# Kernel optimization log

Measured on AMD Instinct MI355X. Metric: run time of the kernel, lower is better.

Reference implementation:

```python
import jax, jax.numpy as jnp
import numpy as np

B, L, D = 4, 2048, 1024
H, DK, DV = 4, 256, 256
CHUNK = 32
MIN_FLOOR, MAX_FLOOR = 0.01, 0.1
EPS = 1e-5


def _l2norm(x):
    return x * jax.lax.rsqrt(jnp.sum(x * x, -1, keepdims=True) + 1e-6)


def _causal_dwconv(x, w):
    # x: [b, L, C], w: [C, k] -> depthwise causal 1d conv
    b, l, c = x.shape
    k = w.shape[-1]
    xt = jnp.transpose(x, (0, 2, 1))
    y = jax.lax.conv_general_dilated(xt, w[:, None, :], (1,), [(k - 1, 0)],
                                     dimension_numbers=('NCH', 'OIH', 'NCH'),
                                     feature_group_count=c)
    return jnp.transpose(y, (0, 2, 1))


def _delta_rule_chunkwise(q, k, v, beta, chunk=CHUNK):
    # q,k: [b,h,L,dk]; v: [b,h,L,dv]; beta: [b,h,L]; L % chunk == 0
    b, h, l, dk = q.shape
    dv = v.shape[-1]
    q = _l2norm(q)
    k = _l2norm(k)
    v = v * beta[..., None]
    kb = k * beta[..., None]
    n = l // chunk
    resh = lambda t: t.reshape(b, h, n, chunk, t.shape[-1])
    q, k, v, kb = resh(q), resh(k), resh(v), resh(kb)
    tri = jnp.triu(jnp.ones((chunk, chunk), bool))        # incl diag
    strict = jnp.triu(jnp.ones((chunk, chunk), bool), 1)  # excl diag
    att = jnp.where(tri, 0.0, -(kb @ jnp.swapaxes(k, -1, -2)))
    # UT transform: forward substitution building (I - lower)^{-1}
    for i in range(1, chunk):
        upd = jnp.einsum('bhnj,bhnjk->bhnk', att[..., i, :], att)
        att = att.at[..., i, :i].add(upd[..., :i])
    att = att + jnp.eye(chunk, dtype=att.dtype)
    u = att @ v
    w = att @ kb

    def step(S, xs):
        q_i, k_i, u_i, w_i = xs  # [b,h,chunk,d]
        local = jnp.where(strict, 0.0, q_i @ jnp.swapaxes(k_i, -1, -2))
        u_adj = u_i - w_i @ S
        o_i = q_i @ S + local @ u_adj
        return S + jnp.swapaxes(k_i, -1, -2) @ u_adj, o_i

    xs = tuple(jnp.moveaxis(t, 2, 0) for t in (q, k, u, w))
    S0 = jnp.zeros((b, h, dk, dv), q.dtype)
    S, o = jax.lax.scan(step, S0, xs)
    return jnp.moveaxis(o, 0, 2).reshape(b, h, l, dv), S


def _rmsnorm(x, w):
    return x * jax.lax.rsqrt(jnp.mean(x * x, -1, keepdims=True) + EPS) * w


def setup_inputs():
    key = jax.random.key(0)
    ks = jax.random.split(key, 16)
    s = 0.02
    return {
        'hidden_states': jax.random.normal(ks[0], (B, L, D), jnp.float32),
        'W_q': jax.random.normal(ks[1], (D, H * DK), jnp.float32) * s,
        'W_k': jax.random.normal(ks[2], (D, H * DK), jnp.float32) * s,
        'W_v': jax.random.normal(ks[3], (D, H * DV), jnp.float32) * s,
        'W_b': jax.random.normal(ks[4], (D, H), jnp.float32) * s,
        'conv_w_q': jax.random.normal(ks[5], (H * DK, 4), jnp.float32) * 0.3,
        'conv_w_k': jax.random.normal(ks[6], (H * DK, 4), jnp.float32) * 0.3,
        'conv_w_v': jax.random.normal(ks[7], (H * DV, 4), jnp.float32) * 0.3,
        'fir_short_w': jax.random.normal(ks[8], (H, DV, 3), jnp.float32) * 0.1,
        'fir_long_w': jax.random.normal(ks[9], (H, DV, 31), jnp.float32) * 0.1,
        'W_fuse1': jax.random.normal(ks[10], (D + 3 * H * DV, 2 * D), jnp.float32) * s,
        'b_fuse1': jnp.zeros((2 * D,), jnp.float32),
        'W_fuse2': jax.random.normal(ks[11], (2 * D, H * 4), jnp.float32) * s,
        'b_fuse2': jnp.zeros((H * 4,), jnp.float32).at[3::4].set(4.0),
        'others_log_tau': jnp.zeros((H,), jnp.float32),
        'norm_w': jnp.ones((DV,), jnp.float32),
        'W_o': jax.random.normal(ks[12], (H * DV, D), jnp.float32) * s,
    }


def reference(hidden_states, W_q, W_k, W_v, W_b, conv_w_q, conv_w_k, conv_w_v,
              fir_short_w, fir_long_w, W_fuse1, b_fuse1, W_fuse2, b_fuse2,
              others_log_tau, norm_w, W_o):
    b, l, d = hidden_states.shape
    # projections + mandatory short conv (silu activation)
    q = jax.nn.silu(_causal_dwconv(hidden_states @ W_q, conv_w_q))
    k = jax.nn.silu(_causal_dwconv(hidden_states @ W_k, conv_w_k))
    v = jax.nn.silu(_causal_dwconv(hidden_states @ W_v, conv_w_v))
    q = q.reshape(b, l, H, DK)
    k = k.reshape(b, l, H, DK)
    v = v.reshape(b, l, H, DV)
    beta = jax.nn.sigmoid(hidden_states @ W_b)  # [b,l,H]
    delta_out, _ = _delta_rule_chunkwise(
        jnp.transpose(q, (0, 2, 1, 3)), jnp.transpose(k, (0, 2, 1, 3)),
        jnp.transpose(v, (0, 2, 1, 3)), jnp.transpose(beta, (0, 2, 1)))
    delta_out = jnp.transpose(delta_out, (0, 2, 1, 3))  # [b,l,H,DV]
    # depthwise FIR paths on v
    vc = v.reshape(b, l, H * DV)
    fir_s = _causal_dwconv(vc, fir_short_w.reshape(H * DV, -1)).reshape(b, l, H, DV)
    fir_l = _causal_dwconv(vc, fir_long_w.reshape(H * DV, -1)).reshape(b, l, H, DV)
    # fusion gate MLP
    gate_in = jnp.concatenate([hidden_states, fir_s.reshape(b, l, -1),
                               fir_l.reshape(b, l, -1), delta_out.reshape(b, l, -1)], -1)
    hid = jax.nn.gelu(gate_in @ W_fuse1 + b_fuse1, approximate=False)
    logits = (hid @ W_fuse2 + b_fuse2).reshape(b, l, H, 4)
    p_raw = jax.nn.sigmoid(logits[..., 3])
    # token-adaptive context floor
    floor = MIN_FLOOR + (MAX_FLOOR - MIN_FLOOR) * (1.0 - p_raw)
    p_val = (1.0 - floor) * p_raw
    tau = jnp.exp(others_log_tau)  # per-head temperature
    others = jax.nn.softmax(logits[..., :3] / tau[None, None, :, None], -1)
    p_ctx = (1.0 - p_val)[..., None] * others
    o = (p_ctx[..., 0:1] * fir_s + p_ctx[..., 1:2] * fir_l +
         p_ctx[..., 2:3] * delta_out + p_val[..., None] * v)
    o = _rmsnorm(o, norm_w)
    return o.reshape(b, l, H * DV) @ W_o
```

## Files before the change

kernel.cpp:

```cpp
#include <hip/hip_runtime.h>
#include <hip/hip_bf16.h>

#define B_ 4
#define L_ 2048
#define D_ 1024
#define H_ 4
#define DK_ 256
#define DV_ 256
#define NCH 64
#define NTOK 8192

typedef __attribute__((ext_vector_type(8))) short bf16x8;
typedef __attribute__((ext_vector_type(4))) float f32x4;
typedef unsigned int u32;

__device__ __forceinline__ float bu2f(unsigned short u) {
    union { unsigned int i; float f; } x; x.i = ((unsigned int)u) << 16; return x.f;
}
__device__ __forceinline__ unsigned short f2bu(float f) {
    union { __hip_bfloat16 h; unsigned short u; } x; x.h = __float2bfloat16(f); return x.u;
}
#define MFMA16(a, b, c) __builtin_amdgcn_mfma_f32_16x16x32_bf16(a, b, c, 0, 0, 0)

__device__ __forceinline__ void gload16(const void* g, void* l) {
    __builtin_amdgcn_global_load_lds(
        (const __attribute__((address_space(1))) u32*)g,
        (__attribute__((address_space(3))) u32*)l, 16, 0, 0);
}

__global__ __launch_bounds__(256) void k_transpose(const float* __restrict__ in,
                                                   unsigned short* __restrict__ out,
                                                   int K, int N) {
    __shared__ float tile[32][33];
    int k0 = blockIdx.y * 32, n0 = blockIdx.x * 32;
    int tx = threadIdx.x & 31, ty = threadIdx.x >> 5;
#pragma unroll
    for (int r = 0; r < 4; ++r)
        tile[ty + 8 * r][tx] = in[(long)(k0 + ty + 8 * r) * N + n0 + tx];
    __syncthreads();
#pragma unroll
    for (int r = 0; r < 4; ++r)
        out[(long)(n0 + ty + 8 * r) * K + k0 + tx] = f2bu(tile[tx][ty + 8 * r]);
}

__global__ __launch_bounds__(256) void k_padT2(const float* __restrict__ W,
                                               unsigned short* __restrict__ out) {
    long idx = (long)blockIdx.x * 256 + threadIdx.x;
    int n = (int)(idx >> 11), k = (int)(idx & 2047);
    out[idx] = (n < 16) ? f2bu(W[k * 16 + n]) : (unsigned short)0;
}

__global__ __launch_bounds__(256) void k_cvt_hs(const float4* __restrict__ hs4,
                                                unsigned short* __restrict__ gate_in) {
    int idx = blockIdx.x * 256 + threadIdx.x;
    float4 v = hs4[idx];
    int row = idx >> 8;
    int c4 = (idx & 255) * 4;
    ushort4 o;
    o.x = f2bu(v.x); o.y = f2bu(v.y); o.z = f2bu(v.z); o.w = f2bu(v.w);
    *reinterpret_cast<ushort4*>(&gate_in[(long)row * 4096 + c4]) = o;
}

__global__ __launch_bounds__(64) void k_beta(const float* __restrict__ hs,
                                             const float* __restrict__ W_b,
                                             float* __restrict__ beta) {
    int tok = blockIdx.x;
    int lane = threadIdx.x;
    const float* hrow = hs + (long)tok * D_;
    float acc0 = 0, acc1 = 0, acc2 = 0, acc3 = 0;
    for (int c = lane; c < D_; c += 64) {
        float x = hrow[c];
        float4 wb = reinterpret_cast<const float4*>(W_b)[c];
        acc0 += x * wb.x; acc1 += x * wb.y; acc2 += x * wb.z; acc3 += x * wb.w;
    }
#pragma unroll
    for (int off = 32; off; off >>= 1) {
        acc0 += __shfl_down(acc0, off);
        acc1 += __shfl_down(acc1, off);
        acc2 += __shfl_down(acc2, off);
        acc3 += __shfl_down(acc3, off);
    }
    if (lane == 0) {
        int b = tok >> 11, l = tok & 2047;
        beta[((long)(b * H_ + 0)) * L_ + l] = 1.f / (1.f + expf(-acc0));
        beta[((long)(b * H_ + 1)) * L_ + l] = 1.f / (1.f + expf(-acc1));
        beta[((long)(b * H_ + 2)) * L_ + l] = 1.f / (1.f + expf(-acc2));
        beta[((long)(b * H_ + 3)) * L_ + l] = 1.f / (1.f + expf(-acc3));
    }
}

template <int EPI>
__global__ __launch_bounds__(256) void k_gemm(const unsigned short* __restrict__ A, int lda,
                                              const unsigned short* __restrict__ BT, int ldb,
                                              void* __restrict__ Cout, int ldc,
                                              const float* __restrict__ bias,
                                              int K, int gx) {
    __shared__ __align__(16) unsigned short As[128][64];
    __shared__ __align__(16) unsigned short Bs[128][64];
    const int tid = threadIdx.x;
    const int wave = tid >> 6, lane = tid & 63;
    const int wm = wave & 1, wn = wave >> 1;
    const int lr = lane & 15, lg = lane >> 4;
    const int nwg = gridDim.x;
    const int cpx = nwg >> 3;
    const int orig = blockIdx.x;
    const int wg = (orig & 7) * cpx + (orig >> 3);
    const int m0 = (wg / gx) * 128, n0 = (wg % gx) * 128;
    const int srow = wave * 32 + (lane >> 3);
    const int scol = (lane & 7) * 8;
    const unsigned short* Ap = &A[(long)(m0 + srow) * lda + scol];
    const unsigned short* Bp = &BT[(long)(n0 + srow) * ldb + scol];
    unsigned short* AsB = &As[wave * 32][0];
    unsigned short* BsB = &Bs[wave * 32][0];
    f32x4 acc[4][4] = {};
    for (int k0 = 0; k0 < K; k0 += 64) {
#pragma unroll
        for (int g = 0; g < 4; ++g) {
            gload16(Ap + (long)g * 8 * lda + k0, AsB + g * 8 * 64);
            gload16(Bp + (long)g * 8 * ldb + k0, BsB + g * 8 * 64);
        }
        __syncthreads();
#pragma unroll
        for (int ks = 0; ks < 2; ++ks) {
            bf16x8 af[4], bfr[4];
#pragma unroll
            for (int mt = 0; mt < 4; ++mt)
                af[mt] = *reinterpret_cast<const bf16x8*>(&As[wm * 64 + mt * 16 + lr][ks * 32 + lg * 8]);
#pragma unroll
            for (int nt = 0; nt < 4; ++nt)
                bfr[nt] = *reinterpret_cast<const bf16x8*>(&Bs[wn * 64 + nt * 16 + lr][ks * 32 + lg * 8]);
#pragma unroll
            for (int mt = 0; mt < 4; ++mt)
#pragma unroll
                for (int nt = 0; nt < 4; ++nt)
                    acc[mt][nt] = MFMA16(af[mt], bfr[nt], acc[mt][nt]);
        }
        __syncthreads();
    }
#pragma unroll
    for (int mt = 0; mt < 4; ++mt)
#pragma unroll
        for (int nt = 0; nt < 4; ++nt)
#pragma unroll
            for (int r = 0; r < 4; ++r) {
                int row = m0 + wm * 64 + mt * 16 + lg * 4 + r;
                int col = n0 + wn * 64 + nt * 16 + lr;
                float v = acc[mt][nt][r];
                if (EPI == 2) {
                    v += bias[col];
                    v = 0.5f * v * (1.f + erff(v * 0.70710678118f));
                }
                if (EPI == 0)
                    reinterpret_cast<float*>(Cout)[(long)row * ldc + col] = v;
                else
                    reinterpret_cast<unsigned short*>(Cout)[(long)row * ldc + col] = f2bu(v);
            }
}

__global__ __launch_bounds__(256) void k_conv_silu(const unsigned short* __restrict__ QKVp,
                                                   const float* __restrict__ cwq,
                                                   const float* __restrict__ cwk,
                                                   const float* __restrict__ cwv,
                                                   unsigned short* __restrict__ qn,
                                                   unsigned short* __restrict__ kn,
                                                   unsigned short* __restrict__ v_blc) {
    int tok = blockIdx.x;
    int b = tok >> 11, l = tok & 2047;
    int t = threadIdx.x;
    float y[12];
#pragma unroll
    for (int j = 0; j < 12; ++j) {
        int c = t + 256 * j;
        const float* cw = (j < 4) ? &cwq[c * 4] : (j < 8) ? &cwk[(c - 1024) * 4] : &cwv[(c - 2048) * 4];
        float s = 0.f;
#pragma unroll
        for (int jj = 0; jj < 4; ++jj) {
            int tl = l - 3 + jj;
            if (tl >= 0) s += bu2f(QKVp[((long)(b * L_ + tl)) * 3072 + c]) * cw[jj];
        }
        y[j] = s / (1.f + expf(-s));
    }
    float sq[8];
#pragma unroll
    for (int j = 0; j < 8; ++j) sq[j] = y[j] * y[j];
    int wave = t >> 6, lane = t & 63;
#pragma unroll
    for (int off = 32; off; off >>= 1)
#pragma unroll
        for (int j = 0; j < 8; ++j) sq[j] += __shfl_down(sq[j], off);
    __shared__ float red[4][8];
    if (lane == 0)
#pragma unroll
        for (int j = 0; j < 8; ++j) red[wave][j] = sq[j];
    __syncthreads();
    float tot[8];
#pragma unroll
    for (int j = 0; j < 8; ++j) tot[j] = red[0][j] + red[1][j] + red[2][j] + red[3][j];
#pragma unroll
    for (int h = 0; h < 4; ++h) {
        float sc = rsqrtf(tot[h] + 1e-6f);
        qn[((long)(b * H_ + h) * L_ + l) * 256 + t] = f2bu(y[h] * sc);
    }
#pragma unroll
    for (int h = 0; h < 4; ++h) {
        float sc = rsqrtf(tot[4 + h] + 1e-6f);
        kn[((long)(b * H_ + h) * L_ + l) * 256 + t] = f2bu(y[4 + h] * sc);
    }
#pragma unroll
    for (int h = 0; h < 4; ++h)
        v_blc[(long)tok * 1024 + h * 256 + t] = f2bu(y[8 + h]);
}

__global__ __launch_bounds__(256) void k_delta_chunk(const unsigned short* __restrict__ qn,
                                                     const unsigned short* __restrict__ kn,
                                                     const unsigned short* __restrict__ v_blc,
                                                     const float* __restrict__ beta,
                                                     unsigned short* __restrict__ u_buf,
                                                     unsigned short* __restrict__ w_buf,
                                                     unsigned short* __restrict__ local_buf,
                                                     unsigned short* __restrict__ kT_buf) {
    int bid = blockIdx.x;
    int n = bid & 63, bh = bid >> 6;
    int b = bh >> 2, h = bh & 3;
    int t0 = n * 32;
    __shared__ __align__(16) unsigned short k_s[32][264];
    __shared__ __align__(16) unsigned short vbT[256][40];
    __shared__ __align__(16) unsigned short kbT[256][40];
    __shared__ __align__(16) float att[32][33];
    __shared__ __align__(16) unsigned short att_b[32][40];
    __shared__ float bet[32];
    int tid = threadIdx.x, wave = tid >> 6, lane = tid & 63;
    int lr = lane & 15, lg = lane >> 4;

    {
        int row = tid >> 3;
        int cc = (tid & 7) * 32;
        float brow = beta[(long)bh * L_ + t0 + row];
        if ((tid & 7) == 0) bet[row] = brow;
        const uint4* kp = reinterpret_cast<const uint4*>(&kn[((long)bh * L_ + t0 + row) * 256 + cc]);
        const uint4* vp = reinterpret_cast<const uint4*>(&v_blc[((long)(b * L_ + t0 + row)) * 1024 + h * 256 + cc]);
        unsigned short kv[32], vv[32];
#pragma unroll
        for (int g = 0; g < 4; ++g) {
            uint4 x = kp[g];
            *reinterpret_cast<uint4*>(&kv[g * 8]) = x;
            *reinterpret_cast<uint4*>(&k_s[row][cc + g * 8]) = x;
            *reinterpret_cast<uint4*>(&vv[g * 8]) = vp[g];
        }
#pragma unroll
        for (int e = 0; e < 32; ++e) {
            kbT[cc + e][row] = f2bu(bu2f(kv[e]) * brow);
            vbT[cc + e][row] = f2bu(bu2f(vv[e]) * brow);
        }
    }
    __syncthreads();

    {
        unsigned short tmp[32];
#pragma unroll
        for (int t = 0; t < 32; ++t) tmp[t] = k_s[t][tid];
#pragma unroll
        for (int g = 0; g < 4; ++g)
            *reinterpret_cast<uint4*>(&kT_buf[((long)bid * 256 + tid) * 32 + g * 8]) =
                *reinterpret_cast<uint4*>(&tmp[g * 8]);
    }

    {
        int i0 = (wave & 1) * 16, j0 = (wave >> 1) * 16;
        f32x4 G = {0, 0, 0, 0}, S2 = {0, 0, 0, 0};
#pragma unroll
        for (int kk = 0; kk < 8; ++kk) {
            bf16x8 bk = *reinterpret_cast<const bf16x8*>(&k_s[j0 + lr][kk * 32 + lg * 8]);
            bf16x8 ak = *reinterpret_cast<const bf16x8*>(&k_s[i0 + lr][kk * 32 + lg * 8]);
            bf16x8 aq = *reinterpret_cast<const bf16x8*>(&qn[((long)bh * L_ + t0 + i0 + lr) * 256 + kk * 32 + lg * 8]);
            G = MFMA16(ak, bk, G);
            S2 = MFMA16(aq, bk, S2);
        }
#pragma unroll
        for (int r = 0; r < 4; ++r) {
            int i = i0 + lg * 4 + r, j = j0 + lr;
            att[i][j] = (j < i) ? -bet[i] * G[r] : 0.f;
            local_buf[(long)bid * 1024 + i * 32 + j] = f2bu((j <= i) ? S2[r] : 0.f);
        }
    }
    __syncthreads();

    for (int i = 1; i < 32; ++i) {
        float upd = 0.f;
        if (tid < i) {
            for (int j = tid + 1; j < i; ++j) upd += att[i][j] * att[j][tid];
        }
        __syncthreads();
        if (tid < i) att[i][tid] += upd;
        __syncthreads();
    }
    for (int e = tid; e < 1024; e += 256) {
        int i = e >> 5, j = e & 31;
        att_b[i][j] = f2bu(att[i][j] + ((i == j) ? 1.f : 0.f));
    }
    __syncthreads();

    {
        int mt = wave & 1;
        bf16x8 afr = *reinterpret_cast<const bf16x8*>(&att_b[mt * 16 + lr][lg * 8]);
        f32x4 z = {0, 0, 0, 0};
#pragma unroll
        for (int ntt = 0; ntt < 8; ++ntt) {
            int n0c = (wave >> 1) * 128 + ntt * 16;
            bf16x8 bu = *reinterpret_cast<const bf16x8*>(&vbT[n0c + lr][lg * 8]);
            bf16x8 bw = *reinterpret_cast<const bf16x8*>(&kbT[n0c + lr][lg * 8]);
            f32x4 ut = MFMA16(afr, bu, z);
            f32x4 wt = MFMA16(afr, bw, z);
#pragma unroll
            for (int r = 0; r < 4; ++r) {
                int t = mt * 16 + lg * 4 + r, c = n0c + lr;
                u_buf[((long)bid * 32 + t) * 256 + c] = f2bu(ut[r]);
                w_buf[((long)bid * 32 + t) * 256 + c] = f2bu(wt[r]);
            }
        }
    }
}

__global__ __launch_bounds__(256) void k_scan(const unsigned short* __restrict__ qn,
                                              const unsigned short* __restrict__ u_buf,
                                              const unsigned short* __restrict__ w_buf,
                                              const unsigned short* __restrict__ local_buf,
                                              const unsigned short* __restrict__ kT_buf,
                                              unsigned short* __restrict__ gate_in) {
    int bid = blockIdx.x;
    int bh = bid & 15, dvb = bid >> 4;
    int b = bh >> 2, h = bh & 3;
    int dc0 = dvb * 16;
    __shared__ __align__(16) unsigned short Tb[16][264];
    __shared__ __align__(16) unsigned short uaT[16][40];
    const int tid = threadIdx.x, wave = tid >> 6, lane = tid & 63;
    const int lr = lane & 15, lg = lane >> 4;
    const int wi = wave & 1;
    const bool isW = wave < 2;
    const int c0w = wave * 64;
    f32x4 Tacc[4] = {};
    for (int e = tid; e < 16 * 264; e += 256) (&Tb[0][0])[e] = 0;
    const unsigned short* q_bh = qn + (long)bh * L_ * 256;
    const unsigned short* u_bh = u_buf + (long)bh * 64 * 8192;
    const unsigned short* w_bh = w_buf + (long)bh * 64 * 8192;
    const unsigned short* l_bh = local_buf + (long)bh * 64 * 1024;
    const unsigned short* kT_bh = kT_buf + (long)bh * 64 * 8192;
    const unsigned short* wq_base = (isW ? w_bh : q_bh) + (16 * wi + lr) * 256;
    const unsigned short* u_base = u_bh + (16 * wi + lg * 4) * 256 + dc0 + lr;
    const unsigned short* l_base = l_bh + (16 * wi + lr) * 32 + lg * 8;
    const unsigned short* kT_base = kT_bh + (c0w + lr) * 32 + lg * 8;
    bf16x8 wqA[8], kB[4], lA = {};
    float uv[4];
    auto prefetch = [&](int n) {
        long o8 = (long)n * 8192;
#pragma unroll
        for (int kk = 0; kk < 8; ++kk)
            wqA[kk] = *reinterpret_cast<const bf16x8*>(wq_base + o8 + kk * 32 + lg * 8);
#pragma unroll
        for (int cc = 0; cc < 4; ++cc)
            kB[cc] = *reinterpret_cast<const bf16x8*>(kT_base + o8 + cc * 512);
        if (isW) {
#pragma unroll
            for (int r = 0; r < 4; ++r) uv[r] = bu2f(u_base[o8 + r * 256]);
        } else {
            lA = *reinterpret_cast<const bf16x8*>(l_base + (long)n * 1024);
        }
    };
    prefetch(0);
    __syncthreads();
    for (int n = 0; n < 64; ++n) {
        f32x4 P0 = {0, 0, 0, 0}, P1 = {0, 0, 0, 0};
#pragma unroll
        for (int kk = 0; kk < 8; kk += 2) {
            bf16x8 t0 = *reinterpret_cast<const bf16x8*>(&Tb[lr][kk * 32 + lg * 8]);
            bf16x8 t1 = *reinterpret_cast<const bf16x8*>(&Tb[lr][(kk + 1) * 32 + lg * 8]);
            P0 = MFMA16(wqA[kk], t0, P0);
            P1 = MFMA16(wqA[kk + 1], t1, P1);
        }
        f32x4 P;
#pragma unroll
        for (int r = 0; r < 4; ++r) P[r] = P0[r] + P1[r];
        if (isW) {
#pragma unroll
            for (int r = 0; r < 4; ++r)
                uaT[lr][16 * wi + lg * 4 + r] = f2bu(uv[r] - P[r]);
        }
        bf16x8 kBc[4];
#pragma unroll
        for (int cc = 0; cc < 4; ++cc) kBc[cc] = kB[cc];
        bf16x8 lAc = lA;
        if (n + 1 < 64) prefetch(n + 1);
        __syncthreads();
        bf16x8 uaA = *reinterpret_cast<const bf16x8*>(&uaT[lr][lg * 8]);
        if (!isW) {
            f32x4 O = MFMA16(lAc, uaA, P);
#pragma unroll
            for (int r = 0; r < 4; ++r) {
                long row = (long)b * L_ + n * 32 + 16 * wi + lg * 4 + r;
                gate_in[row * 4096 + 3072 + h * 256 + dc0 + lr] = f2bu(O[r]);
            }
        }
#pragma unroll
        for (int cc = 0; cc < 4; ++cc)
            Tacc[cc] = MFMA16(uaA, kBc[cc], Tacc[cc]);
#pragma unroll
        for (int cc = 0; cc < 4; ++cc)
#pragma unroll
            for (int r = 0; r < 4; ++r)
                Tb[lg * 4 + r][c0w + cc * 16 + lr] = f2bu(Tacc[cc][r]);
        __syncthreads();
    }
}

__global__ __launch_bounds__(256) void k_fir(const unsigned short* __restrict__ v_blc,
                                             const float* __restrict__ ws3,
                                             const float* __restrict__ wl31,
                                             unsigned short* __restrict__ gate_in) {
    __shared__ unsigned short xs[94][256];
    int b = blockIdx.y, tt = blockIdx.x * 64, c0 = blockIdx.z * 256;
    int tid = threadIdx.x;
    for (int r = 0; r < 94; ++r) {
        int t = tt - 30 + r;
        xs[r][tid] = (t >= 0) ? v_blc[((long)(b * L_ + t)) * 1024 + c0 + tid] : (unsigned short)0;
    }
    int c = c0 + tid;
    float wl[31], ws[3];
#pragma unroll
    for (int j = 0; j < 31; ++j) wl[j] = wl31[(long)c * 31 + j];
#pragma unroll
    for (int j = 0; j < 3; ++j) ws[j] = ws3[(long)c * 3 + j];
    __syncthreads();
    for (int t = 0; t < 64; ++t) {
        float accl = 0.f, accs = 0.f;
#pragma unroll
        for (int j = 0; j < 31; ++j) accl += bu2f(xs[t + j][tid]) * wl[j];
#pragma unroll
        for (int j = 0; j < 3; ++j) accs += bu2f(xs[t + 28 + j][tid]) * ws[j];
        long row = (long)b * L_ + tt + t;
        gate_in[row * 4096 + 1024 + c] = f2bu(accs);
        gate_in[row * 4096 + 2048 + c] = f2bu(accl);
    }
}

__global__ __launch_bounds__(256) void k_gate(const float* __restrict__ logits_pre,
                                              const float* __restrict__ b_fuse2,
                                              const float* __restrict__ log_tau,
                                              const float* __restrict__ norm_w,
                                              const unsigned short* __restrict__ gate_in,
                                              const unsigned short* __restrict__ v_blc,
                                              unsigned short* __restrict__ o_norm) {
    int tok = blockIdx.x;
    int tid = threadIdx.x;
    __shared__ float lg_s[16];
    __shared__ float red[4][4];
    if (tid < 16) lg_s[tid] = logits_pre[(long)tok * 128 + tid] + b_fuse2[tid];
    __syncthreads();
    float o[4];
#pragma unroll
    for (int h = 0; h < 4; ++h) {
        float l0 = lg_s[h * 4 + 0], l1 = lg_s[h * 4 + 1], l2 = lg_s[h * 4 + 2], l3 = lg_s[h * 4 + 3];
        float praw = 1.f / (1.f + expf(-l3));
        float fl_ = 0.01f + 0.09f * (1.f - praw);
        float pval = (1.f - fl_) * praw;
        float itau = expf(-log_tau[h]);
        float a0 = l0 * itau, a1 = l1 * itau, a2 = l2 * itau;
        float m = fmaxf(a0, fmaxf(a1, a2));
        float e0 = expf(a0 - m), e1 = expf(a1 - m), e2 = expf(a2 - m);
        float inv = (1.f - pval) / (e0 + e1 + e2);
        long base = (long)tok * 4096;
        float fs = bu2f(gate_in[base + 1024 + h * 256 + tid]);
        float flv = bu2f(gate_in[base + 2048 + h * 256 + tid]);
        float dd = bu2f(gate_in[base + 3072 + h * 256 + tid]);
        float vv = bu2f(v_blc[(long)tok * 1024 + h * 256 + tid]);
        o[h] = e0 * inv * fs + e1 * inv * flv + e2 * inv * dd + pval * vv;
    }
    int wave = tid >> 6, lane = tid & 63;
    float s[4];
#pragma unroll
    for (int h = 0; h < 4; ++h) s[h] = o[h] * o[h];
#pragma unroll
    for (int off = 32; off; off >>= 1)
#pragma unroll
        for (int h = 0; h < 4; ++h) s[h] += __shfl_down(s[h], off);
    if (lane == 0)
#pragma unroll
        for (int h = 0; h < 4; ++h) red[wave][h] = s[h];
    __syncthreads();
#pragma unroll
    for (int h = 0; h < 4; ++h) {
        float tot = red[0][h] + red[1][h] + red[2][h] + red[3][h];
        float sc = rsqrtf(tot * (1.f / 256.f) + 1e-5f);
        o_norm[(long)tok * 1024 + h * 256 + tid] = f2bu(o[h] * sc * norm_w[tid]);
    }
}

extern "C" void kernel_launch(void* const* d_in, const int* in_sizes, int n_in,
                              void* d_out, int out_size, void* d_ws, size_t ws_size,
                              hipStream_t stream) {
    const float* hs = (const float*)d_in[0];
    const float* W_q = (const float*)d_in[1];
    const float* W_k = (const float*)d_in[2];
    const float* W_v = (const float*)d_in[3];
    const float* W_b = (const float*)d_in[4];
    const float* cwq = (const float*)d_in[5];
    const float* cwk = (const float*)d_in[6];
    const float* cwv = (const float*)d_in[7];
    const float* fir_s_w = (const float*)d_in[8];
    const float* fir_l_w = (const float*)d_in[9];
    const float* W_f1 = (const float*)d_in[10];
    const float* b_f1 = (const float*)d_in[11];
    const float* W_f2 = (const float*)d_in[12];
    const float* b_f2 = (const float*)d_in[13];
    const float* log_tau = (const float*)d_in[14];
    const float* norm_w = (const float*)d_in[15];
    const float* W_o = (const float*)d_in[16];

    char* ws = (char*)d_ws;
    size_t off = 0;
    auto alloc = [&](size_t bytes) { size_t o = off; off += (bytes + 255) & ~(size_t)255; return o; };
    unsigned short* gate_in = (unsigned short*)(ws + alloc((size_t)NTOK * 4096 * 2));
    unsigned short* QKVp    = (unsigned short*)(ws + alloc((size_t)NTOK * 3072 * 2));
    unsigned short* WqkvT   = (unsigned short*)(ws + alloc((size_t)3072 * 1024 * 2));
    unsigned short* Wf1T    = (unsigned short*)(ws + alloc((size_t)2048 * 4096 * 2));
    unsigned short* WoT     = (unsigned short*)(ws + alloc((size_t)1024 * 1024 * 2));
    unsigned short* Wf2Tp   = (unsigned short*)(ws + alloc((size_t)128 * 2048 * 2));
    float*          beta    = (float*)(ws + alloc((size_t)16 * 2048 * 4));
    unsigned short* qn      = (unsigned short*)(ws + alloc((size_t)16 * 2048 * 256 * 2));
    unsigned short* kn      = (unsigned short*)(ws + alloc((size_t)16 * 2048 * 256 * 2));
    unsigned short* v_blc   = (unsigned short*)(ws + alloc((size_t)NTOK * 1024 * 2));
    unsigned short* u_buf   = (unsigned short*)(ws + alloc((size_t)16 * 64 * 8192 * 2));
    unsigned short* w_buf   = (unsigned short*)(ws + alloc((size_t)16 * 64 * 8192 * 2));
    unsigned short* locb    = (unsigned short*)(ws + alloc((size_t)16 * 64 * 1024 * 2));
    unsigned short* kT_buf  = (unsigned short*)(ws + alloc((size_t)16 * 64 * 8192 * 2));
    float*          logits  = (float*)(ws + alloc((size_t)NTOK * 128 * 4));
    unsigned short* o_norm  = (unsigned short*)(ws + alloc((size_t)NTOK * 1024 * 2));
    unsigned short* hid     = QKVp;

    k_transpose<<<dim3(32, 32), 256, 0, stream>>>(W_q, WqkvT, 1024, 1024);
    k_transpose<<<dim3(32, 32), 256, 0, stream>>>(W_k, WqkvT + (size_t)1024 * 1024, 1024, 1024);
    k_transpose<<<dim3(32, 32), 256, 0, stream>>>(W_v, WqkvT + (size_t)2048 * 1024, 1024, 1024);
    k_transpose<<<dim3(64, 128), 256, 0, stream>>>(W_f1, Wf1T, 4096, 2048);
    k_transpose<<<dim3(32, 32), 256, 0, stream>>>(W_o, WoT, 1024, 1024);
    k_padT2<<<1024, 256, 0, stream>>>(W_f2, Wf2Tp);
    k_cvt_hs<<<8192, 256, 0, stream>>>((const float4*)hs, gate_in);
    k_beta<<<8192, 64, 0, stream>>>(hs, W_b, beta);
    k_gemm<1><<<24 * 64, 256, 0, stream>>>(gate_in, 4096, WqkvT, 1024, QKVp, 3072, nullptr,
                                           1024, 24);
    k_conv_silu<<<8192, 256, 0, stream>>>(QKVp, cwq, cwk, cwv, qn, kn, v_blc);
    k_delta_chunk<<<1024, 256, 0, stream>>>(qn, kn, v_blc, beta, u_buf, w_buf, locb, kT_buf);
    k_scan<<<256, 256, 0, stream>>>(qn, u_buf, w_buf, locb, kT_buf, gate_in);
    k_fir<<<dim3(32, 4, 4), 256, 0, stream>>>(v_blc, fir_s_w, fir_l_w, gate_in);
    k_gemm<2><<<16 * 64, 256, 0, stream>>>(gate_in, 4096, Wf1T, 4096, hid, 2048, b_f1,
                                           4096, 16);
    k_gemm<0><<<1 * 64, 256, 0, stream>>>(hid, 2048, Wf2Tp, 2048, logits, 128, nullptr,
                                          2048, 1);
    k_gate<<<8192, 256, 0, stream>>>(logits, b_f2, log_tau, norm_w, gate_in, v_blc, o_norm);
    k_gemm<0><<<8 * 64, 256, 0, stream>>>(o_norm, 1024, WoT, 1024, (float*)d_out, 1024, nullptr,
                                          1024, 8);
}
```

Baseline: 788.1 us.

## Add 4-stage LDS ring pipeline with swizzle to GEMMs, 256x256 tile for fuse1

After: 834.2 us. 1.06x slower.

```diff
diff --git a/kernel.cpp b/kernel.cpp
--- a/kernel.cpp
+++ b/kernel.cpp
@@ -27,6 +27,13 @@
         (const __attribute__((address_space(1))) u32*)g,
         (__attribute__((address_space(3))) u32*)l, 16, 0, 0);
 }
+
+#define RBARRIER() { asm volatile("" ::: "memory"); __builtin_amdgcn_s_barrier(); \
+                     asm volatile("" ::: "memory"); }
+#define RING_WAIT(s, S) { \
+    if ((s) + 3 < (S))      { asm volatile("s_waitcnt vmcnt(8)" ::: "memory"); } \
+    else if ((s) + 2 < (S)) { asm volatile("s_waitcnt vmcnt(4)" ::: "memory"); } \
+    else if ((s) + 1 < (S)) { asm volatile("s_waitcnt vmcnt(0)" ::: "memory"); } }
 
 __global__ __launch_bounds__(256) void k_transpose(const float* __restrict__ in,
                                                    unsigned short* __restrict__ out,
@@ -90,53 +97,152 @@
 }
 
 template <int EPI>
+__global__ __launch_bounds__(512, 2) void k_gemm256(const unsigned short* __restrict__ A, int lda,
+                                                    const unsigned short* __restrict__ BT, int ldb,
+                                                    void* __restrict__ Cout, int ldc,
+                                                    const float* __restrict__ bias,
+                                                    int K, int gx) {
+    __shared__ __align__(16) unsigned short As[4][256][32];
+    __shared__ __align__(16) unsigned short Bs[4][256][32];
+    const int tid = threadIdx.x;
+    const int wave = tid >> 6, lane = tid & 63;
+    const int wm = wave >> 2, wn = wave & 3;
+    const int lr = lane & 15, lg = lane >> 4;
+    const int nwg = gridDim.x, cpx = nwg >> 3, orig = blockIdx.x;
+    const int wg = (orig & 7) * cpx + (orig >> 3);
+    const int m0 = (wg / gx) * 256, n0 = (wg % gx) * 256;
+    const int srow = lane >> 2;
+    const int sgrp = ((lane & 3) ^ ((lane >> 4) & 3)) * 8;
+    const unsigned short* Ag0 = A + (long)(m0 + wave * 16 + srow) * lda + sgrp;
+    const unsigned short* Ag1 = Ag0 + (long)128 * lda;
+    const unsigned short* Bg0 = BT + (long)(n0 + wave * 16 + srow) * ldb + sgrp;
+    const unsigned short* Bg1 = Bg0 + (long)128 * ldb;
+    const int S = K >> 5;
+    f32x4 acc[8][4] = {};
+    const int gsw = (lg ^ ((lr >> 2) & 3)) * 8;
+
+#define STG_A2(sidx) { int sl_ = (sidx) & 3; long ko_ = (long)(sidx) * 32; \
+    gload16(Ag0 + ko_, &As[sl_][wave * 16][0]); \
+    gload16(Ag1 + ko_, &As[sl_][128 + wave * 16][0]); }
+#define STG_B2(sidx) { int sl_ = (sidx) & 3; long ko_ = (long)(sidx) * 32; \
+    gload16(Bg0 + ko_, &Bs[sl_][wave * 16][0]); \
+    gload16(Bg1 + ko_, &Bs[sl_][128 + wave * 16][0]); }
+
+    STG_A2(0) STG_B2(0) STG_A2(1) STG_B2(1) STG_A2(2) STG_B2(2)
+    asm volatile("s_waitcnt vmcnt(8)" ::: "memory");
+    RBARRIER()
+
+    for (int s = 0; s < S; ++s) {
+        const int sl = s & 3;
+        const bool more = (s + 3) < S;
+        bf16x8 b[4], a[4];
+        if (more) STG_A2(s + 3)
+#pragma unroll
+        for (int nt = 0; nt < 4; ++nt)
+            b[nt] = *reinterpret_cast<const bf16x8*>(&Bs[sl][wn * 64 + nt * 16 + lr][gsw]);
+#pragma unroll
+        for (int i = 0; i < 4; ++i)
+            a[i] = *reinterpret_cast<const bf16x8*>(&As[sl][wm * 128 + i * 16 + lr][gsw]);
+        __builtin_amdgcn_s_setprio(1);
+#pragma unroll
+        for (int i = 0; i < 4; ++i)
+#pragma unroll
+            for (int nt = 0; nt < 4; ++nt)
+                acc[i][nt] = MFMA16(a[i], b[nt], acc[i][nt]);
+        __builtin_amdgcn_s_setprio(0);
+        RBARRIER()
+        if (more) STG_B2(s + 3)
+#pragma unroll
+        for (int i = 0; i < 4; ++i)
+            a[i] = *reinterpret_cast<const bf16x8*>(&As[sl][wm * 128 + (4 + i) * 16 + lr][gsw]);
+        __builtin_amdgcn_s_setprio(1);
+#pragma unroll
+        for (int i = 0; i < 4; ++i)
+#pragma unroll
+            for (int nt = 0; nt < 4; ++nt)
+                acc[4 + i][nt] = MFMA16(a[i], b[nt], acc[4 + i][nt]);
+        __builtin_amdgcn_s_setprio(0);
+        RING_WAIT(s, S)
+        RBARRIER()
+    }
+#undef STG_A2
+#undef STG_B2
+#pragma unroll
+    for (int mt = 0; mt < 8; ++mt)
+#pragma unroll
+        for (int nt = 0; nt < 4; ++nt)
+#pragma unroll
+            for (int r = 0; r < 4; ++r) {
+                int row = m0 + wm * 128 + mt * 16 + lg * 4 + r;
+                int col = n0 + wn * 64 + nt * 16 + lr;
+                float v = acc[mt][nt][r];
+                if (EPI == 2) {
+                    v += bias[col];
+                    v = 0.5f * v * (1.f + erff(v * 0.70710678118f));
+                }
+                if (EPI == 0)
+                    reinterpret_cast<float*>(Cout)[(long)row * ldc + col] = v;
+                else
+                    reinterpret_cast<unsigned short*>(Cout)[(long)row * ldc + col] = f2bu(v);
+            }
+}
+
+template <int EPI>
 __global__ __launch_bounds__(256) void k_gemm(const unsigned short* __restrict__ A, int lda,
                                               const unsigned short* __restrict__ BT, int ldb,
                                               void* __restrict__ Cout, int ldc,
                                               const float* __restrict__ bias,
                                               int K, int gx) {
-    __shared__ __align__(16) unsigned short As[128][64];
-    __shared__ __align__(16) unsigned short Bs[128][64];
+    __shared__ __align__(16) unsigned short As[4][128][32];
+    __shared__ __align__(16) unsigned short Bs[4][128][32];
     const int tid = threadIdx.x;
     const int wave = tid >> 6, lane = tid & 63;
     const int wm = wave & 1, wn = wave >> 1;
     const int lr = lane & 15, lg = lane >> 4;
-    const int nwg = gridDim.x;
-    const int cpx = nwg >> 3;
-    const int orig = blockIdx.x;
+    const int nwg = gridDim.x, cpx = nwg >> 3, orig = blockIdx.x;
     const int wg = (orig & 7) * cpx + (orig >> 3);
     const int m0 = (wg / gx) * 128, n0 = (wg % gx) * 128;
-    const int srow = wave * 32 + (lane >> 3);
-    const int scol = (lane & 7) * 8;
-    const unsigned short* Ap = &A[(long)(m0 + srow) * lda + scol];
-    const unsigned short* Bp = &BT[(long)(n0 + srow) * ldb + scol];
-    unsigned short* AsB = &As[wave * 32][0];
-    unsigned short* BsB = &Bs[wave * 32][0];
+    const int srow = lane >> 2;
+    const int sgrp = ((lane & 3) ^ ((lane >> 4) & 3)) * 8;
+    const unsigned short* Ag0 = A + (long)(m0 + wave * 16 + srow) * lda + sgrp;
+    const unsigned short* Ag1 = Ag0 + (long)64 * lda;
+    const unsigned short* Bg0 = BT + (long)(n0 + wave * 16 + srow) * ldb + sgrp;
+    const unsigned short* Bg1 = Bg0 + (long)64 * ldb;
+    const int S = K >> 5;
     f32x4 acc[4][4] = {};
-    for (int k0 = 0; k0 < K; k0 += 64) {
-#pragma unroll
-        for (int g = 0; g < 4; ++g) {
-            gload16(Ap + (long)g * 8 * lda + k0, AsB + g * 8 * 64);
-            gload16(Bp + (long)g * 8 * ldb + k0, BsB + g * 8 * 64);
-        }
-        __syncthreads();
-#pragma unroll
-        for (int ks = 0; ks < 2; ++ks) {
-            bf16x8 af[4], bfr[4];
-#pragma unroll
-            for (int mt = 0; mt < 4; ++mt)
-                af[mt] = *reinterpret_cast<const bf16x8*>(&As[wm * 64 + mt * 16 + lr][ks * 32 + lg * 8]);
+    const int gsw = (lg ^ ((lr >> 2) & 3)) * 8;
+
+#define STG128(sidx) { int sl_ = (sidx) & 3; long ko_ = (long)(sidx) * 32; \
+    gload16(Ag0 + ko_, &As[sl_][wave * 16][0]); \
+    gload16(Ag1 + ko_, &As[sl_][64 + wave * 16][0]); \
+    gload16(Bg0 + ko_, &Bs[sl_][wave * 16][0]); \
+    gload16(Bg1 + ko_, &Bs[sl_][64 + wave * 16][0]); }
+
+    STG128(0) STG128(1) STG128(2)
+    asm volatile("s_waitcnt vmcnt(8)" ::: "memory");
+    RBARRIER()
+
+    for (int s = 0; s < S; ++s) {
+        const int sl = s & 3;
+        if (s + 3 < S) STG128(s + 3)
+        bf16x8 a[4], b[4];
+#pragma unroll
+        for (int mt = 0; mt < 4; ++mt)
+            a[mt] = *reinterpret_cast<const bf16x8*>(&As[sl][wm * 64 + mt * 16 + lr][gsw]);
+#pragma unroll
+        for (int nt = 0; nt < 4; ++nt)
+            b[nt] = *reinterpret_cast<const bf16x8*>(&Bs[sl][wn * 64 + nt * 16 + lr][gsw]);
+        __builtin_amdgcn_s_setprio(1);
+#pragma unroll
+        for (int mt = 0; mt < 4; ++mt)
 #pragma unroll
             for (int nt = 0; nt < 4; ++nt)
-                bfr[nt] = *reinterpret_cast<const bf16x8*>(&Bs[wn * 64 + nt * 16 + lr][ks * 32 + lg * 8]);
-#pragma unroll
-            for (int mt = 0; mt < 4; ++mt)
-#pragma unroll
-                for (int nt = 0; nt < 4; ++nt)
-                    acc[mt][nt] = MFMA16(af[mt], bfr[nt], acc[mt][nt]);
-        }
-        __syncthreads();
-    }
+                acc[mt][nt] = MFMA16(a[mt], b[nt], acc[mt][nt]);
+        __builtin_amdgcn_s_setprio(0);
+        RING_WAIT(s, S)
+        RBARRIER()
+    }
+#undef STG128
 #pragma unroll
     for (int mt = 0; mt < 4; ++mt)
 #pragma unroll
@@ -550,8 +656,8 @@
     k_delta_chunk<<<1024, 256, 0, stream>>>(qn, kn, v_blc, beta, u_buf, w_buf, locb, kT_buf);
     k_scan<<<256, 256, 0, stream>>>(qn, u_buf, w_buf, locb, kT_buf, gate_in);
     k_fir<<<dim3(32, 4, 4), 256, 0, stream>>>(v_blc, fir_s_w, fir_l_w, gate_in);
-    k_gemm<2><<<16 * 64, 256, 0, stream>>>(gate_in, 4096, Wf1T, 4096, hid, 2048, b_f1,
-                                           4096, 16);
+    k_gemm256<2><<<32 * 8, 512, 0, stream>>>(gate_in, 4096, Wf1T, 4096, hid, 2048, b_f1,
+                                             4096, 8);
     k_gemm<0><<<1 * 64, 256, 0, stream>>>(hid, 2048, Wf2Tp, 2048, logits, 128, nullptr,
                                           2048, 1);
     k_gate<<<8192, 256, 0, stream>>>(logits, b_f2, log_tau, norm_w, gate_in, v_blc, o_norm);
```
